# Optimization experiments

Measured on AMD Instinct MI355X. Metric: run time of the kernel, lower is better.

Reference implementation:

```python
import jax, jax.numpy as jnp
import numpy as np

RBF_DIM = 16
RBF_DMAX = 10.0
EPS = 1e-8


def _rbf(d):
    # GVP-style radial basis featurization: [..., RBF_DIM]
    mu = jnp.linspace(0.0, RBF_DMAX, RBF_DIM)
    sigma = RBF_DMAX / RBF_DIM
    return jnp.exp(-(((d[..., None] - mu) / sigma) ** 2))


def _norm_no_nan(x):
    return jnp.sqrt(jnp.clip(jnp.sum(x * x, axis=-1), EPS, None))


def setup_inputs() -> dict:
    key = jax.random.key(0)
    ks = jax.random.split(key, 16)
    N, Eu = 100000, 800000
    D_node, D_edge = 128, 64
    n_a, n_e = 16, 5
    s_t = jax.random.normal(ks[0], (N, D_node), jnp.float32)
    x_t = jax.random.normal(ks[1], (N, 3), jnp.float32) * 3.0
    v_t = jax.random.normal(ks[2], (N, 4, 3), jnp.float32)
    e_t = jax.random.normal(ks[3], (2 * Eu, D_edge), jnp.float32)
    dst_lig_x = x_t + jax.random.normal(ks[4], (N, 3), jnp.float32)
    dst_lig_a = jax.random.uniform(ks[5], (N, n_a), jnp.float32)
    dst_lig_e = jax.random.uniform(ks[6], (Eu, n_e), jnp.float32)
    # symmetric edge list: first Eu edges are "upper", second Eu their mirror
    src_u = jax.random.randint(ks[7], (Eu,), 0, N)
    dst_u = jax.random.randint(ks[8], (Eu,), 0, N)
    edge_src = jnp.concatenate([src_u, dst_u]).astype(jnp.int64)
    edge_dst = jnp.concatenate([dst_u, src_u]).astype(jnp.int64)
    # node residual MLP params (in = rbf + one-hot lig_a + s_t)
    din_n = RBF_DIM + n_a + D_node
    W1 = jax.random.normal(ks[9], (din_n, D_node), jnp.float32) / np.sqrt(din_n)
    b1 = jnp.zeros((D_node,), jnp.float32)
    W2 = jax.random.normal(ks[10], (D_node, D_node), jnp.float32) / np.sqrt(D_node)
    b2 = jnp.zeros((D_node,), jnp.float32)
    # edge residual MLP params (in = e_t + lig_e pred + rbf)
    din_e = D_edge + n_e + RBF_DIM
    We = jax.random.normal(ks[11], (din_e, D_edge), jnp.float32) / np.sqrt(din_e)
    be = jnp.zeros((D_edge,), jnp.float32)
    return {"s_t": s_t, "x_t": x_t, "v_t": v_t, "e_t": e_t,
            "dst_lig_x": dst_lig_x, "dst_lig_a": dst_lig_a, "dst_lig_e": dst_lig_e,
            "edge_src": edge_src, "edge_dst": edge_dst,
            "W1": W1, "b1": b1, "W2": W2, "b2": b2, "We": We, "be": be}


def reference(s_t, x_t, v_t, e_t, dst_lig_x, dst_lig_a, dst_lig_e,
              edge_src, edge_dst, W1, b1, W2, b2, We, be):
    # ---- node residual (lig_x generated -> RBF of |x_pred - x_t|; lig_a generated -> pred) ----
    x_diff = dst_lig_x - x_t                      # [N,3]
    dij = _norm_no_nan(x_diff)                    # [N]
    node_in = jnp.concatenate([_rbf(dij), dst_lig_a, s_t], axis=-1)
    h = jax.nn.silu(node_in @ W1 + b1)
    node_res = jax.nn.silu(h @ W2 + b2)
    node_out = s_t + node_res
    # overwrite last vector channel with unit displacement
    v_out = v_t.at[:, -1, :].set(x_diff / dij[:, None])
    # ---- lig_to_lig edge residual on upper edges, mirrored to lower edges ----
    Eu = edge_src.shape[0] // 2
    su, du = edge_src[:Eu], edge_dst[:Eu]
    d_t = _norm_no_nan(x_t[su] - x_t[du])         # current distances
    d_1 = _norm_no_nan(dst_lig_x[su] - dst_lig_x[du])  # predicted distances
    d_input = _rbf(d_1) - _rbf(d_t)               # [Eu, RBF_DIM]
    e_u = e_t[:Eu]
    edge_in = jnp.concatenate([e_u, dst_lig_e, d_input], axis=-1)
    edge_res = jax.nn.silu(edge_in @ We + be)
    feats = e_u + edge_res
    # original scatters feats into both upper-mask and ~upper-mask slots
    e_out = jnp.concatenate([feats, feats], axis=0)
    return node_out, v_out, e_out
```

## Files before the change

### kernel.cpp

```cpp
#include <hip/hip_runtime.h>
#include <math.h>

typedef short bf16x8 __attribute__((ext_vector_type(8)));
typedef float f32x4 __attribute__((ext_vector_type(4)));

__device__ __forceinline__ float silu_f(float x) {
  return x / (1.0f + __expf(-x));
}
__device__ __forceinline__ unsigned short f2bf(float x) {
  union { float f; unsigned u; } v; v.f = x;
  unsigned r = v.u + 0x7FFFu + ((v.u >> 16) & 1u);
  return (unsigned short)(r >> 16);
}
__device__ __forceinline__ float bf2f(unsigned short h) {
  union { unsigned u; float f; } v; v.u = ((unsigned)h) << 16; return v.f;
}

__global__ __launch_bounds__(256)
void prep_kernel(const float* __restrict__ W1, const float* __restrict__ W2,
                 const float* __restrict__ We, unsigned short* __restrict__ ws)
{
  int i = blockIdx.x * 256 + threadIdx.x;
  if (i < 6144) {
    int col = i / 96, k = i - col * 96;
    float v = (k < 85) ? We[k * 64 + col] : 0.0f;
    ws[i] = f2bf(v);
  }
  int j = i - 6144;
  if (j >= 0 && j < 20480) {
    int col = j / 160, k = j - col * 160;
    ws[6144 + j] = f2bf(W1[k * 128 + col]);
  }
  int l = i - 26624;
  if (l >= 0 && l < 16384) {
    int col = l >> 7, k = l & 127;
    ws[26624 + l] = f2bf(W2[k * 128 + col]);
  }
}

__global__ __launch_bounds__(256, 4)
void node_kernel(const float* __restrict__ s_t,
                 const float* __restrict__ x_t,
                 const float* __restrict__ v_t,
                 const float* __restrict__ dst_lig_x,
                 const float* __restrict__ dst_lig_a,
                 const unsigned short* __restrict__ w1t, const float* __restrict__ b1,
                 const unsigned short* __restrict__ w2t, const float* __restrict__ b2,
                 float* __restrict__ node_out, float* __restrict__ v_out,
                 int N)
{
  __shared__ unsigned short A1[64][168];
  __shared__ unsigned short H [64][136];
  __shared__ float xd[64][4];
  const int t = threadIdx.x;
  const int row0 = blockIdx.x * 64;
  const int w = t >> 6, lane = t & 63;

  #pragma unroll
  for (int p = 0; p < 8; ++p) {
    int i = p * 256 + t;
    int row = i >> 5, q = i & 31;
    if (row0 + row < N) {
      const float4 v = *reinterpret_cast<const float4*>(&s_t[(size_t)(row0 + row) * 128 + q * 4]);
      uint2 pk;
      pk.x = f2bf(v.x) | ((unsigned)f2bf(v.y) << 16);
      pk.y = f2bf(v.z) | ((unsigned)f2bf(v.w) << 16);
      *reinterpret_cast<uint2*>(&A1[row][32 + q * 4]) = pk;
    }
  }
  if (t < 64) {
    int row = row0 + t;
    if (row < N) {
      float dx = dst_lig_x[row*3+0] - x_t[row*3+0];
      float dy = dst_lig_x[row*3+1] - x_t[row*3+1];
      float dz = dst_lig_x[row*3+2] - x_t[row*3+2];
      float dij = sqrtf(fmaxf(dx*dx + dy*dy + dz*dz, 1e-8f));
      xd[t][0] = dx; xd[t][1] = dy; xd[t][2] = dz; xd[t][3] = dij;
    }
  }
  __syncthreads();
  #pragma unroll
  for (int p = 0; p < 4; ++p) {
    int i = p * 256 + t;
    int el = i >> 4, m = i & 15;
    int row = row0 + el;
    if (row < N) {
      float dij = xd[el][3];
      float tt = (dij - 0.66666667f * (float)m) * 1.6f;
      A1[el][m]      = f2bf(__expf(-tt * tt));
      A1[el][16 + m] = f2bf(dst_lig_a[(size_t)row * 16 + m]);
      if (m < 12) {
        float val = (m < 9) ? v_t[(size_t)row * 12 + m] : xd[el][m - 9] / dij;
        __builtin_nontemporal_store(val, &v_out[(size_t)row * 12 + m]);
      }
    }
  }
  __syncthreads();

  const int mb = (w & 1) * 32;
  const int nb = (w >> 1) * 64;

  f32x4 acc[2][4] = {};
  #pragma unroll 1
  for (int ks = 0; ks < 5; ++ks) {
    const int ko = ks * 32 + ((lane >> 4) << 3);
    bf16x8 af[2], bfr[4];
    #pragma unroll
    for (int m = 0; m < 2; ++m)
      af[m] = *reinterpret_cast<const bf16x8*>(&A1[mb + m*16 + (lane & 15)][ko]);
    #pragma unroll
    for (int n = 0; n < 4; ++n)
      bfr[n] = *reinterpret_cast<const bf16x8*>(&w1t[(size_t)(nb + n*16 + (lane & 15)) * 160 + ko]);
    #pragma unroll
    for (int m = 0; m < 2; ++m)
      #pragma unroll
      for (int n = 0; n < 4; ++n)
        acc[m][n] = __builtin_amdgcn_mfma_f32_16x16x32_bf16(af[m], bfr[n], acc[m][n], 0, 0, 0);
  }
  #pragma unroll
  for (int n = 0; n < 4; ++n) {
    float bb = b1[nb + n*16 + (lane & 15)];
    #pragma unroll
    for (int m = 0; m < 2; ++m) {
      int r0 = mb + m*16 + ((lane >> 4) << 2);
      int c  = nb + n*16 + (lane & 15);
      #pragma unroll
      for (int r = 0; r < 4; ++r)
        H[r0 + r][c] = f2bf(silu_f(acc[m][n][r] + bb));
    }
  }
  __syncthreads();

  f32x4 acc2[2][4] = {};
  #pragma unroll 1
  for (int ks = 0; ks < 4; ++ks) {
    const int ko = ks * 32 + ((lane >> 4) << 3);
    bf16x8 af[2], bfr[4];
    #pragma unroll
    for (int m = 0; m < 2; ++m)
      af[m] = *reinterpret_cast<const bf16x8*>(&H[mb + m*16 + (lane & 15)][ko]);
    #pragma unroll
    for (int n = 0; n < 4; ++n)
      bfr[n] = *reinterpret_cast<const bf16x8*>(&w2t[(size_t)(nb + n*16 + (lane & 15)) * 128 + ko]);
    #pragma unroll
    for (int m = 0; m < 2; ++m)
      #pragma unroll
      for (int n = 0; n < 4; ++n)
        acc2[m][n] = __builtin_amdgcn_mfma_f32_16x16x32_bf16(af[m], bfr[n], acc2[m][n], 0, 0, 0);
  }
  #pragma unroll
  for (int n = 0; n < 4; ++n) {
    float bb = b2[nb + n*16 + (lane & 15)];
    #pragma unroll
    for (int m = 0; m < 2; ++m) {
      int r0 = mb + m*16 + ((lane >> 4) << 2);
      int c  = nb + n*16 + (lane & 15);
      #pragma unroll
      for (int r = 0; r < 4; ++r) {
        int row = row0 + r0 + r;
        if (row < N) {
          float o = bf2f(A1[r0 + r][32 + c]) + silu_f(acc2[m][n][r] + bb);
          __builtin_nontemporal_store(o, &node_out[(size_t)row * 128 + c]);
        }
      }
    }
  }
}

__global__ __launch_bounds__(256, 4)
void edge_kernel(const float* __restrict__ e_t,
                 const float* __restrict__ x_t,
                 const float* __restrict__ dst_lig_x,
                 const float* __restrict__ dst_lig_e,
                 const int* __restrict__ edge_src,
                 const int* __restrict__ edge_dst,
                 const unsigned short* __restrict__ wet, const float* __restrict__ be,
                 float* __restrict__ e_out0, float* __restrict__ e_out1,
                 int Eu)
{
  __shared__ unsigned short A[64][104];
  __shared__ float dd[64][2];
  const int t = threadIdx.x;
  const int e0 = blockIdx.x * 64;
  const int w = t >> 6, lane = t & 63;

  #pragma unroll
  for (int p = 0; p < 8; ++p) {
    int i = p * 256 + t;
    int row = i >> 5, cp = i & 31;
    if (e0 + row < Eu) {
      const float2 v = *reinterpret_cast<const float2*>(&e_t[(size_t)(e0 + row) * 64 + cp * 2]);
      unsigned pk = f2bf(v.x) | ((unsigned)f2bf(v.y) << 16);
      *reinterpret_cast<unsigned*>(&A[row][cp * 2]) = pk;
    }
  }
  if (t < 128) {
    int el = t >> 1, which = t & 1;
    int e = e0 + el;
    if (e < Eu) {
      int su = edge_src[e], du = edge_dst[e];
      const float* base = which ? dst_lig_x : x_t;
      float u0 = base[su*3+0] - base[du*3+0];
      float u1 = base[su*3+1] - base[du*3+1];
      float u2 = base[su*3+2] - base[du*3+2];
      dd[el][which] = sqrtf(fmaxf(u0*u0 + u1*u1 + u2*u2, 1e-8f));
    }
  }
  #pragma unroll
  for (int q = 0; q < 2; ++q) {
    int i = q * 256 + t;
    if (i < 320) {
      int el = i / 5, c = i - el * 5;
      if (e0 + el < Eu) A[el][64 + c] = f2bf(dst_lig_e[(size_t)(e0 + el) * 5 + c]);
    }
  }
  #pragma unroll
  for (int q = 0; q < 3; ++q) {
    int i = q * 256 + t;
    if (i < 704) { int el = i / 11, c = i - el * 11; A[el][85 + c] = 0; }
  }
  __syncthreads();
  #pragma unroll
  for (int q = 0; q < 4; ++q) {
    int i = q * 256 + t;
    int el = i >> 4, m = i & 15;
    if (e0 + el < Eu) {
      float dt_ = dd[el][0], d1_ = dd[el][1];
      float mu = 0.66666667f * (float)m;
      float a1 = (d1_ - mu) * 1.6f, a2 = (dt_ - mu) * 1.6f;
      A[el][69 + m] = f2bf(__expf(-a1*a1) - __expf(-a2*a2));
    }
  }
  __syncthreads();

  const int mb = (w & 1) * 32;
  const int nb = (w >> 1) * 32;

  f32x4 acc[2][2] = {};
  #pragma unroll 1
  for (int ks = 0; ks < 3; ++ks) {
    const int ko = ks * 32 + ((lane >> 4) << 3);
    bf16x8 af[2], bfr[2];
    #pragma unroll
    for (int m = 0; m < 2; ++m)
      af[m] = *reinterpret_cast<const bf16x8*>(&A[mb + m*16 + (lane & 15)][ko]);
    #pragma unroll
    for (int n = 0; n < 2; ++n)
      bfr[n] = *reinterpret_cast<const bf16x8*>(&wet[(size_t)(nb + n*16 + (lane & 15)) * 96 + ko]);
    #pragma unroll
    for (int m = 0; m < 2; ++m)
      #pragma unroll
      for (int n = 0; n < 2; ++n)
        acc[m][n] = __builtin_amdgcn_mfma_f32_16x16x32_bf16(af[m], bfr[n], acc[m][n], 0, 0, 0);
  }
  #pragma unroll
  for (int n = 0; n < 2; ++n) {
    float bb = be[nb + n*16 + (lane & 15)];
    #pragma unroll
    for (int m = 0; m < 2; ++m) {
      int r0 = mb + m*16 + ((lane >> 4) << 2);
      int c  = nb + n*16 + (lane & 15);
      #pragma unroll
      for (int r = 0; r < 4; ++r) {
        size_t eidx = (size_t)e0 + r0 + r;
        if ((int)eidx < Eu) {
          float feat = bf2f(A[r0 + r][c]) + silu_f(acc[m][n][r] + bb);
          __builtin_nontemporal_store(feat, &e_out0[eidx * 64 + c]);
          __builtin_nontemporal_store(feat, &e_out1[eidx * 64 + c]);
        }
      }
    }
  }
}

extern "C" void kernel_launch(void* const* d_in, const int* in_sizes, int n_in,
                              void* d_out, int out_size, void* d_ws, size_t ws_size,
                              hipStream_t stream) {
  const float* s_t       = (const float*)d_in[0];
  const float* x_t       = (const float*)d_in[1];
  const float* v_t       = (const float*)d_in[2];
  const float* e_t       = (const float*)d_in[3];
  const float* dst_lig_x = (const float*)d_in[4];
  const float* dst_lig_a = (const float*)d_in[5];
  const float* dst_lig_e = (const float*)d_in[6];
  const int*   edge_src  = (const int*)d_in[7];
  const int*   edge_dst  = (const int*)d_in[8];
  const float* W1        = (const float*)d_in[9];
  const float* b1        = (const float*)d_in[10];
  const float* W2        = (const float*)d_in[11];
  const float* b2        = (const float*)d_in[12];
  const float* We        = (const float*)d_in[13];
  const float* be        = (const float*)d_in[14];

  const int N  = in_sizes[0] / 128;
  const int Eu = in_sizes[3] / 128;

  float* out      = (float*)d_out;
  float* node_out = out;
  float* v_out    = out + (size_t)N * 128;
  float* e_out0   = v_out + (size_t)N * 12;
  float* e_out1   = e_out0 + (size_t)Eu * 64;

  unsigned short* wsp = (unsigned short*)d_ws;
  unsigned short* wet = wsp;
  unsigned short* w1t = wsp + 6144;
  unsigned short* w2t = wsp + 26624;

  prep_kernel<<<168, 256, 0, stream>>>(W1, W2, We, wsp);

  node_kernel<<<(N + 63) / 64, 256, 0, stream>>>(
      s_t, x_t, v_t, dst_lig_x, dst_lig_a, w1t, b1, w2t, b2,
      node_out, v_out, N);

  edge_kernel<<<(Eu + 63) / 64, 256, 0, stream>>>(
      e_t, x_t, dst_lig_x, dst_lig_e, edge_src, edge_dst, wet, be,
      e_out0, e_out1, Eu);
}
```

Measured before the change: 281.3 us.

## Enlarge edge tile to 128 rows, drop syncs, use nontemporal vector loads

```diff
diff --git a/kernel.cpp b/kernel.cpp
--- a/kernel.cpp
+++ b/kernel.cpp
@@ -3,6 +3,9 @@
 
 typedef short bf16x8 __attribute__((ext_vector_type(8)));
 typedef float f32x4 __attribute__((ext_vector_type(4)));
+typedef float fvec4 __attribute__((ext_vector_type(4)));
+
+#define EBK 128
 
 __device__ __forceinline__ float silu_f(float x) {
   return x / (1.0f + __expf(-x));
@@ -51,7 +54,6 @@
 {
   __shared__ unsigned short A1[64][168];
   __shared__ unsigned short H [64][136];
-  __shared__ float xd[64][4];
   const int t = threadIdx.x;
   const int row0 = blockIdx.x * 64;
   const int w = t >> 6, lane = t & 63;
@@ -61,36 +63,33 @@
     int i = p * 256 + t;
     int row = i >> 5, q = i & 31;
     if (row0 + row < N) {
-      const float4 v = *reinterpret_cast<const float4*>(&s_t[(size_t)(row0 + row) * 128 + q * 4]);
+      const fvec4 v = __builtin_nontemporal_load(
+          reinterpret_cast<const fvec4*>(&s_t[(size_t)(row0 + row) * 128 + q * 4]));
       uint2 pk;
       pk.x = f2bf(v.x) | ((unsigned)f2bf(v.y) << 16);
       pk.y = f2bf(v.z) | ((unsigned)f2bf(v.w) << 16);
       *reinterpret_cast<uint2*>(&A1[row][32 + q * 4]) = pk;
     }
   }
-  if (t < 64) {
-    int row = row0 + t;
+  #pragma unroll
+  for (int p = 0; p < 4; ++p) {
+    int i = p * 256 + t;
+    int el = i >> 4, m = i & 15;
+    int row = row0 + el;
     if (row < N) {
       float dx = dst_lig_x[row*3+0] - x_t[row*3+0];
       float dy = dst_lig_x[row*3+1] - x_t[row*3+1];
       float dz = dst_lig_x[row*3+2] - x_t[row*3+2];
       float dij = sqrtf(fmaxf(dx*dx + dy*dy + dz*dz, 1e-8f));
-      xd[t][0] = dx; xd[t][1] = dy; xd[t][2] = dz; xd[t][3] = dij;
-    }
-  }
-  __syncthreads();
-  #pragma unroll
-  for (int p = 0; p < 4; ++p) {
-    int i = p * 256 + t;
-    int el = i >> 4, m = i & 15;
-    int row = row0 + el;
-    if (row < N) {
-      float dij = xd[el][3];
       float tt = (dij - 0.66666667f * (float)m) * 1.6f;
       A1[el][m]      = f2bf(__expf(-tt * tt));
       A1[el][16 + m] = f2bf(dst_lig_a[(size_t)row * 16 + m]);
       if (m < 12) {
-        float val = (m < 9) ? v_t[(size_t)row * 12 + m] : xd[el][m - 9] / dij;
+        float val;
+        if (m < 9)       val = v_t[(size_t)row * 12 + m];
+        else if (m == 9) val = dx / dij;
+        else if (m == 10)val = dy / dij;
+        else             val = dz / dij;
         __builtin_nontemporal_store(val, &v_out[(size_t)row * 12 + m]);
       }
     }
@@ -178,88 +177,90 @@
                  float* __restrict__ e_out0, float* __restrict__ e_out1,
                  int Eu)
 {
-  __shared__ unsigned short A[64][104];
-  __shared__ float dd[64][2];
+  __shared__ unsigned short A[EBK][104];
   const int t = threadIdx.x;
-  const int e0 = blockIdx.x * 64;
+  const int e0 = blockIdx.x * EBK;
   const int w = t >> 6, lane = t & 63;
 
   #pragma unroll
   for (int p = 0; p < 8; ++p) {
     int i = p * 256 + t;
-    int row = i >> 5, cp = i & 31;
+    int row = i >> 4, cq = i & 15;
     if (e0 + row < Eu) {
-      const float2 v = *reinterpret_cast<const float2*>(&e_t[(size_t)(e0 + row) * 64 + cp * 2]);
-      unsigned pk = f2bf(v.x) | ((unsigned)f2bf(v.y) << 16);
-      *reinterpret_cast<unsigned*>(&A[row][cp * 2]) = pk;
-    }
-  }
-  if (t < 128) {
-    int el = t >> 1, which = t & 1;
-    int e = e0 + el;
+      const fvec4 v = __builtin_nontemporal_load(
+          reinterpret_cast<const fvec4*>(&e_t[(size_t)(e0 + row) * 64 + cq * 4]));
+      uint2 pk;
+      pk.x = f2bf(v.x) | ((unsigned)f2bf(v.y) << 16);
+      pk.y = f2bf(v.z) | ((unsigned)f2bf(v.w) << 16);
+      *reinterpret_cast<uint2*>(&A[row][cq * 4]) = pk;
+    }
+  }
+  {
+    const int el = t >> 1, which = t & 1;
+    const int e = e0 + el;
+    float dcur = 0.0f;
     if (e < Eu) {
       int su = edge_src[e], du = edge_dst[e];
       const float* base = which ? dst_lig_x : x_t;
       float u0 = base[su*3+0] - base[du*3+0];
       float u1 = base[su*3+1] - base[du*3+1];
       float u2 = base[su*3+2] - base[du*3+2];
-      dd[el][which] = sqrtf(fmaxf(u0*u0 + u1*u1 + u2*u2, 1e-8f));
-    }
-  }
-  #pragma unroll
-  for (int q = 0; q < 2; ++q) {
+      dcur = sqrtf(fmaxf(u0*u0 + u1*u1 + u2*u2, 1e-8f));
+    }
+    float doth = __shfl_xor(dcur, 1);
+    float dt_ = which ? doth : dcur;
+    float d1_ = which ? dcur : doth;
+    if (e < Eu) {
+      #pragma unroll
+      for (int q = 0; q < 8; ++q) {
+        int m = which * 8 + q;
+        float mu = 0.66666667f * (float)m;
+        float a1 = (d1_ - mu) * 1.6f, a2 = (dt_ - mu) * 1.6f;
+        A[el][69 + m] = f2bf(__expf(-a1*a1) - __expf(-a2*a2));
+      }
+    }
+  }
+  #pragma unroll
+  for (int q = 0; q < 3; ++q) {
     int i = q * 256 + t;
-    if (i < 320) {
+    if (i < EBK * 5) {
       int el = i / 5, c = i - el * 5;
       if (e0 + el < Eu) A[el][64 + c] = f2bf(dst_lig_e[(size_t)(e0 + el) * 5 + c]);
     }
   }
   #pragma unroll
-  for (int q = 0; q < 3; ++q) {
+  for (int q = 0; q < 6; ++q) {
     int i = q * 256 + t;
-    if (i < 704) { int el = i / 11, c = i - el * 11; A[el][85 + c] = 0; }
+    if (i < EBK * 11) { int el = i / 11, c = i - el * 11; A[el][85 + c] = 0; }
   }
   __syncthreads();
-  #pragma unroll
-  for (int q = 0; q < 4; ++q) {
-    int i = q * 256 + t;
-    int el = i >> 4, m = i & 15;
-    if (e0 + el < Eu) {
-      float dt_ = dd[el][0], d1_ = dd[el][1];
-      float mu = 0.66666667f * (float)m;
-      float a1 = (d1_ - mu) * 1.6f, a2 = (dt_ - mu) * 1.6f;
-      A[el][69 + m] = f2bf(__expf(-a1*a1) - __expf(-a2*a2));
-    }
-  }
-  __syncthreads();
-
-  const int mb = (w & 1) * 32;
-  const int nb = (w >> 1) * 32;
-
-  f32x4 acc[2][2] = {};
+
+  const int mb = w * 32;
+
+  f32x4 acc[2][4] = {};
   #pragma unroll 1
   for (int ks = 0; ks < 3; ++ks) {
     const int ko = ks * 32 + ((lane >> 4) << 3);
-    bf16x8 af[2], bfr[2];
+    bf16x8 af[2], bfr[4];
     #pragma unroll
     for (int m = 0; m < 2; ++m)
       af[m] = *reinterpret_cast<const bf16x8*>(&A[mb + m*16 + (lane & 15)][ko]);
     #pragma unroll
-    for (int n = 0; n < 2; ++n)
-      bfr[n] = *reinterpret_cast<const bf16x8*>(&wet[(size_t)(nb + n*16 + (lane & 15)) * 96 + ko]);
-    #pragma unroll
-    for (int m = 0; m < 2; ++m)
-      #pragma unroll
-      for (int n = 0; n < 2; ++n)
+    for (int n = 0; n < 4; ++n)
+      bfr[n] = *reinterpret_cast<const bf16x8*>(&wet[(size_t)(n*16 + (lane & 15)) * 96 + ko]);
+    #pragma unroll
+    for (int m = 0; m < 2; ++m)
+      #pragma unroll
+      for (int n = 0; n < 4; ++n)
         acc[m][n] = __builtin_amdgcn_mfma_f32_16x16x32_bf16(af[m], bfr[n], acc[m][n], 0, 0, 0);
   }
   #pragma unroll
-  for (int n = 0; n < 2; ++n) {
-    float bb = be[nb + n*16 + (lane & 15)];
+  for (int n = 0; n < 4; ++n) {
+    float bb = be[n*16 + (lane & 15)];
     #pragma unroll
     for (int m = 0; m < 2; ++m) {
       int r0 = mb + m*16 + ((lane >> 4) << 2);
-      int c  = nb + n*16 + (lane & 15);
+      int c  = n*16 + (lane & 15);
       #pragma unroll
       for (int r = 0; r < 4; ++r) {
         size_t eidx = (size_t)e0 + r0 + r;
@@ -308,11 +309,11 @@
 
   prep_kernel<<<168, 256, 0, stream>>>(W1, W2, We, wsp);
 
+  edge_kernel<<<(Eu + EBK - 1) / EBK, 256, 0, stream>>>(
+      e_t, x_t, dst_lig_x, dst_lig_e, edge_src, edge_dst, wet, be,
+      e_out0, e_out1, Eu);
+
   node_kernel<<<(N + 63) / 64, 256, 0, stream>>>(
       s_t, x_t, v_t, dst_lig_x, dst_lig_a, w1t, b1, w2t, b2,
       node_out, v_out, N);
-
-  edge_kernel<<<(Eu + 63) / 64, 256, 0, stream>>>(
-      e_t, x_t, dst_lig_x, dst_lig_e, edge_src, edge_dst, wet, be,
-      e_out0, e_out1, Eu);
-}
+}
```

Measured after the change: 255.7 us. 9.1% less time.
